# Performance work log

Measured on AMD Instinct MI355X. Metric: run time of the kernel, lower is better.

## Reference

```python
import jax, jax.numpy as jnp
import numpy as np

AH, AW, AL = 7, 7, 7  # aligned_height, aligned_width, aligned_length


def setup_inputs() -> dict:
    key = jax.random.key(0)
    kf, kb, kh, kw, kl = jax.random.split(key, 5)
    B, C, H, W, L = 2, 128, 64, 64, 32
    N = 256
    scale = jnp.float32(0.125)  # stride-8 backbone; image space 512x512x256
    features = jax.random.normal(kf, (B, C, H, W, L), dtype=jnp.float32)
    b = jax.random.randint(kb, (N,), 0, B).astype(jnp.float32)
    hh = jax.random.uniform(kh, (N, 2), minval=0.0, maxval=H / 0.125 - 1.0)
    ww = jax.random.uniform(kw, (N, 2), minval=0.0, maxval=W / 0.125 - 1.0)
    ll = jax.random.uniform(kl, (N, 2), minval=0.0, maxval=L / 0.125 - 1.0)
    rois = jnp.stack([b,
                      jnp.min(hh, 1), jnp.min(ww, 1), jnp.min(ll, 1),
                      jnp.max(hh, 1), jnp.max(ww, 1), jnp.max(ll, 1)], axis=1)
    return {"features": features, "rois": rois, "scale": scale}


def _roi_align_3d(features, rois, scale):
    B, C, H, W, L = features.shape
    dt = features.dtype
    b = rois[:, 0].astype(jnp.int32)
    # roi corners in feature coordinates
    h1, w1, l1 = rois[:, 1] * scale, rois[:, 2] * scale, rois[:, 3] * scale
    h2, w2, l2 = rois[:, 4] * scale, rois[:, 5] * scale, rois[:, 6] * scale
    roi_h = jnp.maximum(h2 - h1 + 1.0, 0.0)
    roi_w = jnp.maximum(w2 - w1 + 1.0, 0.0)
    roi_l = jnp.maximum(l2 - l1 + 1.0, 0.0)
    # one sample per bin at inclusive grid points (legacy RoIAlign style)
    gh = h1[:, None] + (roi_h / (AH - 1))[:, None] * jnp.arange(AH, dtype=dt)  # [N,AH]
    gw = w1[:, None] + (roi_w / (AW - 1))[:, None] * jnp.arange(AW, dtype=dt)  # [N,AW]
    gl = l1[:, None] + (roi_l / (AL - 1))[:, None] * jnp.arange(AL, dtype=dt)  # [N,AL]
    gh = jnp.clip(gh, 0.0, H - 1)[:, :, None, None]   # [N,AH,1,1]
    gw = jnp.clip(gw, 0.0, W - 1)[:, None, :, None]   # [N,1,AW,1]
    gl = jnp.clip(gl, 0.0, L - 1)[:, None, None, :]   # [N,1,1,AL]

    h0 = jnp.floor(gh); w0 = jnp.floor(gw); l0 = jnp.floor(gl)
    fh, fw, fl = gh - h0, gw - w0, gl - l0
    h0i = h0.astype(jnp.int32); w0i = w0.astype(jnp.int32); l0i = l0.astype(jnp.int32)
    h1i = jnp.minimum(h0i + 1, H - 1)
    w1i = jnp.minimum(w0i + 1, W - 1)
    l1i = jnp.minimum(l0i + 1, L - 1)
    bi = b[:, None, None, None]

    def g(hi, wi, li):
        # advanced indexing -> [N,AH,AW,AL,C]
        return features[bi, :, hi, wi, li]

    fh_, fw_, fl_ = fh[..., None], fw[..., None], fl[..., None]
    out = (g(h0i, w0i, l0i) * (1 - fh_) * (1 - fw_) * (1 - fl_)
         + g(h0i, w0i, l1i) * (1 - fh_) * (1 - fw_) * fl_
         + g(h0i, w1i, l0i) * (1 - fh_) * fw_ * (1 - fl_)
         + g(h0i, w1i, l1i) * (1 - fh_) * fw_ * fl_
         + g(h1i, w0i, l0i) * fh_ * (1 - fw_) * (1 - fl_)
         + g(h1i, w0i, l1i) * fh_ * (1 - fw_) * fl_
         + g(h1i, w1i, l0i) * fh_ * fw_ * (1 - fl_)
         + g(h1i, w1i, l1i) * fh_ * fw_ * fl_)
    return jnp.transpose(out, (0, 4, 1, 2, 3))  # [N,C,AH,AW,AL]


def reference(features, rois, scale):
    return _roi_align_3d(features, rois, scale)
```

## Files before the change

kernel.cpp:

```cpp
#include <hip/hip_runtime.h>
#include <cstdint>

#define AH 7
#define AW 7
#define AL 7
constexpr int Bc = 2, Cc = 128, Hc = 64, Wc = 64, Lc = 32, Nc = 256;
constexpr int HWL = Hc * Wc * Lc;
constexpr int WL  = Wc * Lc;
constexpr int VOL = AH * AW * AL;
constexpr int JK  = AW * AL;
constexpr int HALF_E = (Cc / 2) * JK;

__global__ __launch_bounds__(256)
void roialign3d_v2(const float* __restrict__ feat,
                   const float* __restrict__ rois,
                   const float* __restrict__ scale_p,
                   float* __restrict__ out) {
    const int idx = blockIdx.x;
    const int n = idx & 255;
    const int i = idx >> 8;

    const float scale = scale_p[0];
    const float* r = rois + n * 7;
    const int   bi = (int)r[0];
    const float h1 = r[1] * scale, w1 = r[2] * scale, l1 = r[3] * scale;
    const float h2 = r[4] * scale, w2 = r[5] * scale, l2 = r[6] * scale;

    const float sh = fmaxf(h2 - h1 + 1.0f, 0.0f) * (1.0f / (AH - 1));
    const float sw = fmaxf(w2 - w1 + 1.0f, 0.0f) * (1.0f / (AW - 1));
    const float sl = fmaxf(l2 - l1 + 1.0f, 0.0f) * (1.0f / (AL - 1));

    const float gh  = fminf(fmaxf(h1 + sh * (float)i, 0.0f), (float)(Hc - 1));
    const float h0f = floorf(gh);
    const float fh  = gh - h0f;
    const int   h0i = (int)h0f;
    const int   h1i = min(h0i + 1, Hc - 1);
    const float ofh = 1.0f - fh;

    const float* __restrict__ fb  = feat + (size_t)bi * Cc * HWL;
    const float* __restrict__ hp0 = fb + (size_t)h0i * WL;
    const float* __restrict__ hp1 = fb + (size_t)h1i * WL;

    float* __restrict__ outn = out + (size_t)n * Cc * VOL + (size_t)i * JK;

    for (int e = threadIdx.x; e < HALF_E; e += 256) {
        const int k = e % AL;
        const int j = (e / AL) % AW;
        const int c = e / JK;

        const float gw  = fminf(fmaxf(w1 + sw * (float)j, 0.0f), (float)(Wc - 1));
        const float gl  = fminf(fmaxf(l1 + sl * (float)k, 0.0f), (float)(Lc - 1));
        const float w0f = floorf(gw);
        const float l0f = floorf(gl);
        const float fw  = gw - w0f;
        const float fl  = gl - l0f;
        const int   w0i = (int)w0f;
        const int   l0i = (int)l0f;
        const int   w1i = min(w0i + 1, Wc - 1);
        const int   l1i = min(l0i + 1, Lc - 1);

        const size_t cA = (size_t)c * HWL;
        const size_t cB = cA + (size_t)(Cc / 2) * HWL;
        const int r00 = w0i * Lc, r01 = w1i * Lc;

        const float A000 = hp0[cA + r00 + l0i], A001 = hp0[cA + r00 + l1i];
        const float A010 = hp0[cA + r01 + l0i], A011 = hp0[cA + r01 + l1i];
        const float A100 = hp1[cA + r00 + l0i], A101 = hp1[cA + r00 + l1i];
        const float A110 = hp1[cA + r01 + l0i], A111 = hp1[cA + r01 + l1i];
        const float B000 = hp0[cB + r00 + l0i], B001 = hp0[cB + r00 + l1i];
        const float B010 = hp0[cB + r01 + l0i], B011 = hp0[cB + r01 + l1i];
        const float B100 = hp1[cB + r00 + l0i], B101 = hp1[cB + r00 + l1i];
        const float B110 = hp1[cB + r01 + l0i], B111 = hp1[cB + r01 + l1i];

        const float ofl = 1.0f - fl, ofw = 1.0f - fw;
        const float a00 = A000 * ofl + A001 * fl;
        const float a01 = A010 * ofl + A011 * fl;
        const float a10 = A100 * ofl + A101 * fl;
        const float a11 = A110 * ofl + A111 * fl;
        const float b00 = B000 * ofl + B001 * fl;
        const float b01 = B010 * ofl + B011 * fl;
        const float b10 = B100 * ofl + B101 * fl;
        const float b11 = B110 * ofl + B111 * fl;

        const float aa0 = a00 * ofw + a01 * fw;
        const float aa1 = a10 * ofw + a11 * fw;
        const float bb0 = b00 * ofw + b01 * fw;
        const float bb1 = b10 * ofw + b11 * fw;

        const float resA = aa0 * ofh + aa1 * fh;
        const float resB = bb0 * ofh + bb1 * fh;

        const size_t oA = (size_t)c * VOL + (size_t)(j * AL + k);
        outn[oA] = resA;
        outn[oA + (size_t)(Cc / 2) * VOL] = resB;
    }
}

extern "C" void kernel_launch(void* const* d_in, const int* in_sizes, int n_in,
                              void* d_out, int out_size, void* d_ws, size_t ws_size,
                              hipStream_t stream) {
    const float* feat    = (const float*)d_in[0];
    const float* rois    = (const float*)d_in[1];
    const float* scale_p = (const float*)d_in[2];
    float* out = (float*)d_out;

    dim3 grid(Nc * AH);
    dim3 block(256);
    roialign3d_v2<<<grid, block, 0, stream>>>(feat, rois, scale_p, out);
}
```

Measured before the change: 304.8 us.

## Stage full L-rows per channel chunk in LDS with float4 loads before interpolating

Each block now loops over channels in chunks of 8. For each chunk it cooperatively loads the whole 32-float L-rows needed for the two h and two w corners of all 7 w-samples, using coalesced float4 loads, into LDS. The trilinear interpolation then reads from LDS instead of issuing 16 scattered global gathers per output pair. The block index mapping also changes so consecutive blocks share the same ROI, which may improve cache locality. The cost is extra syncthreads, some over-fetch of the L dimension, and redundant loads when w samples coincide.

```diff
diff --git a/kernel.cpp b/kernel.cpp
--- a/kernel.cpp
+++ b/kernel.cpp
@@ -4,21 +4,26 @@
 #define AH 7
 #define AW 7
 #define AL 7
-constexpr int Bc = 2, Cc = 128, Hc = 64, Wc = 64, Lc = 32, Nc = 256;
+constexpr int Cc = 128, Hc = 64, Wc = 64, Lc = 32, Nc = 256;
 constexpr int HWL = Hc * Wc * Lc;
 constexpr int WL  = Wc * Lc;
 constexpr int VOL = AH * AW * AL;
 constexpr int JK  = AW * AL;
-constexpr int HALF_E = (Cc / 2) * JK;
+
+constexpr int CHUNK = 8;
+constexpr int ROWS  = CHUNK * 2 * AW * 2;
+constexpr int RPAD  = 36;
 
 __global__ __launch_bounds__(256)
-void roialign3d_v2(const float* __restrict__ feat,
+void roialign3d_v3(const float* __restrict__ feat,
                    const float* __restrict__ rois,
                    const float* __restrict__ scale_p,
                    float* __restrict__ out) {
+    __shared__ float lds[ROWS * RPAD];
+
     const int idx = blockIdx.x;
-    const int n = idx & 255;
-    const int i = idx >> 8;
+    const int n = idx / AH;
+    const int i = idx % AH;
 
     const float scale = scale_p[0];
     const float* r = rois + n * 7;
@@ -31,68 +36,72 @@
     const float sl = fmaxf(l2 - l1 + 1.0f, 0.0f) * (1.0f / (AL - 1));
 
     const float gh  = fminf(fmaxf(h1 + sh * (float)i, 0.0f), (float)(Hc - 1));
-    const float h0f = floorf(gh);
-    const float fh  = gh - h0f;
-    const int   h0i = (int)h0f;
+    const int   h0i = (int)gh;
+    const float fh  = gh - (float)h0i;
     const int   h1i = min(h0i + 1, Hc - 1);
     const float ofh = 1.0f - fh;
 
-    const float* __restrict__ fb  = feat + (size_t)bi * Cc * HWL;
-    const float* __restrict__ hp0 = fb + (size_t)h0i * WL;
-    const float* __restrict__ hp1 = fb + (size_t)h1i * WL;
+    const float* __restrict__ fb = feat + (size_t)bi * Cc * HWL;
+    float* __restrict__ outni = out + (size_t)n * Cc * VOL + (size_t)i * JK;
 
-    float* __restrict__ outn = out + (size_t)n * Cc * VOL + (size_t)i * JK;
+    for (int c0 = 0; c0 < Cc; c0 += CHUNK) {
+        #pragma unroll
+        for (int p = 0; p < 7; ++p) {
+            const int q    = (int)threadIdx.x + p * 256;
+            const int l4   = q & 7;
+            const int row  = q >> 3;
+            const int cl   = row / 28;
+            const int rr   = row % 28;
+            const int hsel = rr / 14;
+            const int rr2  = rr % 14;
+            const int j    = rr2 >> 1;
+            const int wsel = rr2 & 1;
 
-    for (int e = threadIdx.x; e < HALF_E; e += 256) {
-        const int k = e % AL;
-        const int j = (e / AL) % AW;
-        const int c = e / JK;
+            const float gw = fminf(fmaxf(w1 + sw * (float)j, 0.0f), (float)(Wc - 1));
+            int wv = (int)gw;
+            if (wsel) wv = min(wv + 1, Wc - 1);
+            const int hv = hsel ? h1i : h0i;
 
-        const float gw  = fminf(fmaxf(w1 + sw * (float)j, 0.0f), (float)(Wc - 1));
-        const float gl  = fminf(fmaxf(l1 + sl * (float)k, 0.0f), (float)(Lc - 1));
-        const float w0f = floorf(gw);
-        const float l0f = floorf(gl);
-        const float fw  = gw - w0f;
-        const float fl  = gl - l0f;
-        const int   w0i = (int)w0f;
-        const int   l0i = (int)l0f;
-        const int   w1i = min(w0i + 1, Wc - 1);
-        const int   l1i = min(l0i + 1, Lc - 1);
+            const float4 v = *(const float4*)(fb + (size_t)(c0 + cl) * HWL
+                                              + hv * WL + wv * Lc + l4 * 4);
+            *(float4*)(&lds[row * RPAD + l4 * 4]) = v;
+        }
+        __syncthreads();
 
-        const size_t cA = (size_t)c * HWL;
-        const size_t cB = cA + (size_t)(Cc / 2) * HWL;
-        const int r00 = w0i * Lc, r01 = w1i * Lc;
+        #pragma unroll
+        for (int pass = 0; pass < 2; ++pass) {
+            const int e = (int)threadIdx.x + pass * 256;
+            if (e < CHUNK * JK) {
+                const int k  = e % 7;
+                const int j  = (e / 7) % 7;
+                const int cl = e / 49;
 
-        const float A000 = hp0[cA + r00 + l0i], A001 = hp0[cA + r00 + l1i];
-        const float A010 = hp0[cA + r01 + l0i], A011 = hp0[cA + r01 + l1i];
-        const float A100 = hp1[cA + r00 + l0i], A101 = hp1[cA + r00 + l1i];
-        const float A110 = hp1[cA + r01 + l0i], A111 = hp1[cA + r01 + l1i];
-        const float B000 = hp0[cB + r00 + l0i], B001 = hp0[cB + r00 + l1i];
-        const float B010 = hp0[cB + r01 + l0i], B011 = hp0[cB + r01 + l1i];
-        const float B100 = hp1[cB + r00 + l0i], B101 = hp1[cB + r00 + l1i];
-        const float B110 = hp1[cB + r01 + l0i], B111 = hp1[cB + r01 + l1i];
+                const float gw  = fminf(fmaxf(w1 + sw * (float)j, 0.0f), (float)(Wc - 1));
+                const float gl  = fminf(fmaxf(l1 + sl * (float)k, 0.0f), (float)(Lc - 1));
+                const float fw  = gw - floorf(gw);
+                const int   l0i = (int)gl;
+                const float fl  = gl - (float)l0i;
+                const int   l1i = min(l0i + 1, Lc - 1);
 
-        const float ofl = 1.0f - fl, ofw = 1.0f - fw;
-        const float a00 = A000 * ofl + A001 * fl;
-        const float a01 = A010 * ofl + A011 * fl;
-        const float a10 = A100 * ofl + A101 * fl;
-        const float a11 = A110 * ofl + A111 * fl;
-        const float b00 = B000 * ofl + B001 * fl;
-        const float b01 = B010 * ofl + B011 * fl;
-        const float b10 = B100 * ofl + B101 * fl;
-        const float b11 = B110 * ofl + B111 * fl;
+                const int rbase = cl * 28 + j * 2;
+                const float* r00 = &lds[(rbase +  0) * RPAD];
+                const float* r01 = &lds[(rbase +  1) * RPAD];
+                const float* r10 = &lds[(rbase + 14) * RPAD];
+                const float* r11 = &lds[(rbase + 15) * RPAD];
 
-        const float aa0 = a00 * ofw + a01 * fw;
-        const float aa1 = a10 * ofw + a11 * fw;
-        const float bb0 = b00 * ofw + b01 * fw;
-        const float bb1 = b10 * ofw + b11 * fw;
+                const float ofl = 1.0f - fl, ofw = 1.0f - fw;
+                const float a00 = r00[l0i] * ofl + r00[l1i] * fl;
+                const float a01 = r01[l0i] * ofl + r01[l1i] * fl;
+                const float a10 = r10[l0i] * ofl + r10[l1i] * fl;
+                const float a11 = r11[l0i] * ofl + r11[l1i] * fl;
 
-        const float resA = aa0 * ofh + aa1 * fh;
-        const float resB = bb0 * ofh + bb1 * fh;
+                const float b0 = a00 * ofw + a01 * fw;
+                const float b1 = a10 * ofw + a11 * fw;
 
-        const size_t oA = (size_t)c * VOL + (size_t)(j * AL + k);
-        outn[oA] = resA;
-        outn[oA + (size_t)(Cc / 2) * VOL] = resB;
+                outni[(size_t)(c0 + cl) * VOL + j * AL + k] = b0 * ofh + b1 * fh;
+            }
+        }
+        __syncthreads();
     }
 }
 
@@ -106,5 +115,5 @@
 
     dim3 grid(Nc * AH);
     dim3 block(256);
-    roialign3d_v2<<<grid, block, 0, stream>>>(feat, rois, scale_p, out);
+    roialign3d_v3<<<grid, block, 0, stream>>>(feat, rois, scale_p, out);
 }
```

Result: faster. 267.3 us (-12.3%).
